# Performance work log

Measured on AMD Instinct MI355X. Metric: run time of the kernel, lower is better.

## Reference

```python
import jax, jax.numpy as jnp
import numpy as np

N6 = 524288          # nodes at depth 6 (full-octree batch of 2)
N5 = N6 // 8         # 65536 nodes at depth 5
N4 = N5 // 8         # 8192 nodes at depth 4
EPS = 1e-5           # torch BatchNorm1d default eps


def _pool(x):
    # octree_max_pool on a full octree: 8 contiguous children -> parent max
    n, c = x.shape
    return jnp.max(x.reshape(n // 8, 8, c), axis=1)


def _up(x):
    # octree_upsample on a full octree: each parent broadcast to its 8 children
    return jnp.repeat(x, 8, axis=0)


def _conv1x1_bn_relu(x, w, g, b):
    # Conv1x1 (Linear, no bias) + BatchNorm1d (training-mode batch stats) + ReLU
    y = x @ w                              # [N, Cout]
    m = jnp.mean(y, axis=0)
    v = jnp.var(y, axis=0)                 # biased variance, as in torch BN
    y = (y - m) * jax.lax.rsqrt(v + EPS) * g + b
    return jax.nn.relu(y)


def setup_inputs() -> dict:
    key = jax.random.key(0)
    ks = jax.random.split(key, 8)
    s = 0.02
    return {
        "data0": jax.random.normal(ks[0], (N6, 96), jnp.float32),
        "data1": jax.random.normal(ks[1], (N5, 192), jnp.float32),
        "w01": jax.random.normal(ks[2], (96, 192), jnp.float32) * s,
        "g01": jnp.ones((192,), jnp.float32),
        "b01": jnp.zeros((192,), jnp.float32),
        "w02": jax.random.normal(ks[3], (96, 384), jnp.float32) * s,
        "g02": jnp.ones((384,), jnp.float32),
        "b02": jnp.zeros((384,), jnp.float32),
        "w10": jax.random.normal(ks[4], (192, 96), jnp.float32) * s,
        "g10": jnp.ones((96,), jnp.float32),
        "b10": jnp.zeros((96,), jnp.float32),
        "w12": jax.random.normal(ks[5], (192, 384), jnp.float32) * s,
        "g12": jnp.ones((384,), jnp.float32),
        "b12": jnp.zeros((384,), jnp.float32),
        "depth": 6,
    }


def reference(data0, data1, w01, g01, b01, w02, g02, b02,
              w10, g10, b10, w12, g12, b12, depth):
    # channels = [96, 192, 384]; data0 at depth, data1 at depth-1.
    # out[j] = sum_i TransFunc(channels[i]->channels[j])(data[i], depth-i -> depth-j)
    # j=0 (depth, 96ch):   identity(data0) + upsample(conv10(data1))
    out0 = data0 + _up(_conv1x1_bn_relu(data1, w10, g10, b10))
    # j=1 (depth-1, 192ch): conv01(pool(data0)) + identity(data1)
    p0 = _pool(data0)                      # [N5, 96]
    out1 = _conv1x1_bn_relu(p0, w01, g01, b01) + data1
    # j=2 (depth-2, 384ch): conv02(pool^2(data0)) + conv12(pool(data1))
    out2 = (_conv1x1_bn_relu(_pool(p0), w02, g02, b02)
            + _conv1x1_bn_relu(_pool(data1), w12, g12, b12))
    return (out0, out1, out2)
```

## Files before the change

kernel.cpp:

```cpp
#include <hip/hip_runtime.h>

typedef unsigned short u16;
typedef __attribute__((ext_vector_type(8))) short short8;
typedef __attribute__((ext_vector_type(4))) float f4;
typedef __attribute__((ext_vector_type(4))) unsigned short u16x4;

#define CN6 524288
#define CN5 65536
#define CN4 8192

__device__ inline u16 f2bf(float f){
  unsigned u = __float_as_uint(f);
  return (u16)((u + 0x7FFFu + ((u >> 16) & 1u)) >> 16);
}
__device__ inline float bf2f(u16 h){ return __uint_as_float(((unsigned)h) << 16); }

__device__ inline f4 nt_load4(const float* p){
  return __builtin_nontemporal_load(reinterpret_cast<const f4*>(p));
}
__device__ inline void nt_store4(float* p, f4 v){
  __builtin_nontemporal_store(v, reinterpret_cast<f4*>(p));
}


__global__ __launch_bounds__(256) void k_prep(const float* __restrict__ w10, const float* __restrict__ w01,
                                              const float* __restrict__ w02, const float* __restrict__ w12,
                                              u16* __restrict__ wT10, u16* __restrict__ wT01,
                                              u16* __restrict__ wT02, u16* __restrict__ wT12,
                                              float* __restrict__ stats){
  int i = blockIdx.x * 256 + threadIdx.x;
  if (i < 2112) stats[i] = 0.f;
  if (i < 18432){ int j = i / 192, k = i - j * 192; wT10[i] = f2bf(w10[k * 96 + j]); }
  else if (i < 36864){ int e = i - 18432; int j = e / 96, k = e - j * 96; wT01[e] = f2bf(w01[k * 192 + j]); }
  else if (i < 73728){ int e = i - 36864; int j = e / 96, k = e - j * 96; wT02[e] = f2bf(w02[k * 384 + j]); }
  else if (i < 147456){ int e = i - 73728; int j = e / 192, k = e - j * 192; wT12[e] = f2bf(w12[k * 384 + j]); }
}

__global__ __launch_bounds__(256) void k_gemm10p(const float* __restrict__ d1, const u16* __restrict__ wT10,
                                                 u16* __restrict__ y10, u16* __restrict__ p1){
  __shared__ u16 sm[64 * 200];
  int tid = threadIdx.x, bid = blockIdx.x;

  if (tid < 192){
    int p = tid / 24, c8 = tid - p * 24;
    f4 v0[8], v1[8];
    #pragma unroll
    for (int r = 0; r < 8; r++){
      const float* src = d1 + ((size_t)bid * 64 + p * 8 + r) * 192 + c8 * 8;
      v0[r] = *reinterpret_cast<const f4*>(src);
      v1[r] = *reinterpret_cast<const f4*>(src + 4);
    }
    float mx[8];
    #pragma unroll
    for (int q = 0; q < 4; q++){ mx[q] = v0[0][q]; mx[4 + q] = v1[0][q]; }
    #pragma unroll
    for (int r = 0; r < 8; r++){
      short8 h;
      #pragma unroll
      for (int q = 0; q < 4; q++){
        h[q]     = (short)f2bf(v0[r][q]);
        h[4 + q] = (short)f2bf(v1[r][q]);
        if (r){ mx[q] = fmaxf(mx[q], v0[r][q]); mx[4 + q] = fmaxf(mx[4 + q], v1[r][q]); }
      }
      *reinterpret_cast<short8*>(&sm[(p * 8 + r) * 200 + c8 * 8]) = h;
    }
    short8 hp;
    #pragma unroll
    for (int q = 0; q < 8; q++) hp[q] = (short)f2bf(mx[q]);
    *reinterpret_cast<short8*>(p1 + ((size_t)bid * 8 + p) * 192 + c8 * 8) = hp;
  }
  __syncthreads();

  int lane = tid & 63, wave = tid >> 6;
  int colb = lane & 15;
  int k0 = (lane >> 4) * 8, rgrp = (lane >> 4) * 4;
  int arowl = wave * 16 + colb;
  short8 xf[6];
  #pragma unroll
  for (int s = 0; s < 6; s++) xf[s] = *reinterpret_cast<short8*>(&sm[arowl * 200 + s * 32 + k0]);

  size_t xrow = (size_t)bid * 64 + arowl;
  #pragma unroll
  for (int j = 0; j < 6; j++){
    f4 acc = {0.f, 0.f, 0.f, 0.f};
    const u16* wr = wT10 + (size_t)(j * 16 + colb) * 192 + k0;
    #pragma unroll
    for (int s = 0; s < 6; s++)
      acc = __builtin_amdgcn_mfma_f32_16x16x32_bf16(*reinterpret_cast<const short8*>(wr + s * 32), xf[s], acc, 0, 0, 0);
    u16x4 h;
    #pragma unroll
    for (int r = 0; r < 4; r++) h[r] = f2bf(acc[r]);
    *reinterpret_cast<u16x4*>(y10 + xrow * 96 + j * 16 + rgrp) = h;
  }
}

__global__ __launch_bounds__(192) void k_stats10(const u16* __restrict__ y10, float* __restrict__ stats){
  __shared__ float ls[96], lq[96];
  int tid = threadIdx.x, bid = blockIdx.x;
  if (tid < 96){ ls[tid] = 0.f; lq[tid] = 0.f; }
  __syncthreads();
  int c8 = tid % 12, rl = tid / 12;
  float s1[8], s2[8];
  #pragma unroll
  for (int q = 0; q < 8; q++){ s1[q] = 0.f; s2[q] = 0.f; }
  for (int it = 0; it < 32; it++){
    size_t row = (size_t)bid * 512 + it * 16 + rl;
    short8 h = *reinterpret_cast<const short8*>(y10 + row * 96 + c8 * 8);
    #pragma unroll
    for (int q = 0; q < 8; q++){
      float v = bf2f((u16)h[q]);
      s1[q] += v; s2[q] += v * v;
    }
  }
  #pragma unroll
  for (int q = 0; q < 8; q++){
    atomicAdd(&ls[c8 * 8 + q], s1[q]);
    atomicAdd(&lq[c8 * 8 + q], s2[q]);
  }
  __syncthreads();
  if (tid < 96){ atomicAdd(&stats[tid], ls[tid]); atomicAdd(&stats[1056 + tid], lq[tid]); }
}

__global__ __launch_bounds__(192) void k_out0(const float* __restrict__ d0, const u16* __restrict__ y10,
                                              const float* __restrict__ stats,
                                              const float* __restrict__ g10, const float* __restrict__ b10,
                                              float* __restrict__ out0, u16* __restrict__ p0, u16* __restrict__ p00){
  __shared__ float aL[96], cL[96];
  __shared__ float sp[8][96];
  int tid = threadIdx.x, gp = blockIdx.x;
  if (tid < 96){
    float m = stats[tid] * (1.f / 65536.f);
    float v = stats[1056 + tid] * (1.f / 65536.f) - m * m;
    float a = g10[tid] * rsqrtf(v + 1e-5f);
    aL[tid] = a; cL[tid] = b10[tid] - m * a;
  }
  __syncthreads();

  int p = tid / 24, c4 = tid - p * 24;
  int par = gp * 8 + p;
  u16x4 yb = *reinterpret_cast<const u16x4*>(y10 + (size_t)par * 96 + c4 * 4);
  size_t base = ((size_t)par * 8) * 96 + c4 * 4;

  f4 v[8];
  #pragma unroll
  for (int r = 0; r < 8; r++) v[r] = nt_load4(d0 + base + r * 96);

  f4 yv;
  #pragma unroll
  for (int q = 0; q < 4; q++){
    int c = c4 * 4 + q;
    yv[q] = fmaxf(bf2f((u16)yb[q]) * aL[c] + cL[c], 0.f);
  }
  f4 mx = v[0];
  #pragma unroll
  for (int r = 1; r < 8; r++)
    #pragma unroll
    for (int q = 0; q < 4; q++) mx[q] = fmaxf(mx[q], v[r][q]);

  #pragma unroll
  for (int r = 0; r < 8; r++){
    f4 o;
    #pragma unroll
    for (int q = 0; q < 4; q++) o[q] = v[r][q] + yv[q];
    nt_store4(out0 + base + r * 96, o);
  }

  u16x4 hp;
  #pragma unroll
  for (int q = 0; q < 4; q++) hp[q] = f2bf(mx[q]);
  *reinterpret_cast<u16x4*>(p0 + (size_t)par * 96 + c4 * 4) = hp;
  *reinterpret_cast<f4*>(&sp[p][c4 * 4]) = mx;
  __syncthreads();

  if (tid < 24){
    f4 m = *reinterpret_cast<f4*>(&sp[0][tid * 4]);
    #pragma unroll
    for (int pp = 1; pp < 8; pp++){
      f4 x = *reinterpret_cast<f4*>(&sp[pp][tid * 4]);
      #pragma unroll
      for (int q = 0; q < 4; q++) m[q] = fmaxf(m[q], x[q]);
    }
    u16x4 h;
    #pragma unroll
    for (int q = 0; q < 4; q++) h[q] = f2bf(m[q]);
    *reinterpret_cast<u16x4*>(p00 + (size_t)gp * 96 + tid * 4) = h;
  }
}

template<int Ci, int Co>
__device__ __forceinline__ void stats_body(const u16* __restrict__ x, const u16* __restrict__ wT,
                                           float* __restrict__ sum, float* __restrict__ sq,
                                           int bid, float* ls, float* lq){
  int tid = threadIdx.x;
  for (int t = tid; t < Co; t += 256){ ls[t] = 0.f; lq[t] = 0.f; }
  __syncthreads();
  int lane = tid & 63, wave = tid >> 6;
  int arow = bid * 64 + wave * 16 + (lane & 15);
  int k0 = (lane >> 4) * 8;
  constexpr int KS = Ci / 32;
  short8 af[KS];
  const u16* xr = x + (size_t)arow * Ci + k0;
  #pragma unroll
  for (int s = 0; s < KS; s++) af[s] = *reinterpret_cast<const short8*>(xr + s * 32);
  int colb = lane & 15;
  #pragma unroll 4
  for (int j = 0; j < Co / 16; j++){
    int col = j * 16 + colb;
    f4 acc = {0.f, 0.f, 0.f, 0.f};
    const u16* wr = wT + (size_t)col * Ci + k0;
    #pragma unroll
    for (int s = 0; s < KS; s++)
      acc = __builtin_amdgcn_mfma_f32_16x16x32_bf16(af[s], *reinterpret_cast<const short8*>(wr + s * 32), acc, 0, 0, 0);
    float s1 = acc[0] + acc[1] + acc[2] + acc[3];
    float s2 = acc[0]*acc[0] + acc[1]*acc[1] + acc[2]*acc[2] + acc[3]*acc[3];
    atomicAdd(&ls[col], s1);
    atomicAdd(&lq[col], s2);
  }
  __syncthreads();
  for (int t = tid; t < Co; t += 256){ atomicAdd(&sum[t], ls[t]); atomicAdd(&sq[t], lq[t]); }
}

__global__ __launch_bounds__(256) void k_statsAll(const u16* __restrict__ p0, const u16* __restrict__ p00,
                                                  const u16* __restrict__ p1,
                                                  const u16* __restrict__ wT01, const u16* __restrict__ wT02,
                                                  const u16* __restrict__ wT12, float* __restrict__ stats){
  __shared__ float ls[384], lq[384];
  int bid = blockIdx.x;
  if (bid < 1024)      stats_body<96, 192>(p0,  wT01, stats + 96,  stats + 1056 + 96,  bid,        ls, lq);
  else if (bid < 1152) stats_body<96, 384>(p00, wT02, stats + 288, stats + 1056 + 288, bid - 1024, ls, lq);
  else                 stats_body<192,384>(p1,  wT12, stats + 672, stats + 1056 + 672, bid - 1152, ls, lq);
}

__global__ __launch_bounds__(256) void k_out1(const u16* __restrict__ p0, const u16* __restrict__ wT01,
                                              const float* __restrict__ d1, const float* __restrict__ stats,
                                              const float* __restrict__ g01, const float* __restrict__ b01,
                                              float* __restrict__ out1){
  __shared__ float aL[192], cL[192];
  __shared__ float so[64 * 196];
  int tid = threadIdx.x, bid = blockIdx.x;
  if (tid < 192){
    float m = stats[96 + tid] * (1.f / 65536.f);
    float v = stats[1056 + 96 + tid] * (1.f / 65536.f) - m * m;
    float a = g01[tid] * rsqrtf(v + 1e-5f);
    aL[tid] = a; cL[tid] = b01[tid] - m * a;
  }
  __syncthreads();
  int lane = tid & 63, wave = tid >> 6;
  int colb = lane & 15;
  int k0 = (lane >> 4) * 8, rgrp = (lane >> 4) * 4;
  int rowl = wave * 16 + colb;
  short8 xf[3];
  const u16* xr = p0 + ((size_t)bid * 64 + rowl) * 96 + k0;
  #pragma unroll
  for (int s = 0; s < 3; s++) xf[s] = *reinterpret_cast<const short8*>(xr + s * 32);
  #pragma unroll 4
  for (int j = 0; j < 12; j++){
    int ch0 = j * 16 + rgrp;
    f4 acc = {0.f, 0.f, 0.f, 0.f};
    const u16* wr = wT01 + (size_t)(j * 16 + colb) * 96 + k0;
    #pragma unroll
    for (int s = 0; s < 3; s++)
      acc = __builtin_amdgcn_mfma_f32_16x16x32_bf16(*reinterpret_cast<const short8*>(wr + s * 32), xf[s], acc, 0, 0, 0);
    f4 o;
    #pragma unroll
    for (int r = 0; r < 4; r++){
      int ch = ch0 + r;
      o[r] = fmaxf(acc[r] * aL[ch] + cL[ch], 0.f);
    }
    *reinterpret_cast<f4*>(&so[rowl * 196 + ch0]) = o;
  }
  __syncthreads();
  const float* d1b = d1 + (size_t)bid * 64 * 192;
  float* o1b = out1 + (size_t)bid * 64 * 192;
  #pragma unroll
  for (int i = 0; i < 12; i++){
    int idx = i * 256 + tid;
    int rl = idx / 48, c4 = idx % 48;
    f4 y = *reinterpret_cast<f4*>(&so[rl * 196 + c4 * 4]);
    int off = rl * 192 + c4 * 4;
    f4 g = nt_load4(d1b + off);
    f4 o;
    #pragma unroll
    for (int q = 0; q < 4; q++) o[q] = y[q] + g[q];
    nt_store4(o1b + off, o);
  }
}

__global__ __launch_bounds__(256) void k_out2(const u16* __restrict__ p00, const u16* __restrict__ p1,
                                              const u16* __restrict__ wT02, const u16* __restrict__ wT12,
                                              const float* __restrict__ stats,
                                              const float* __restrict__ g02, const float* __restrict__ b02,
                                              const float* __restrict__ g12, const float* __restrict__ b12,
                                              float* __restrict__ out2){
  __shared__ float a2[384], c2[384], a1[384], c1[384];
  __shared__ float so[32 * 392];
  int tid = threadIdx.x, bid = blockIdx.x;
  for (int t = tid; t < 384; t += 256){
    float m = stats[288 + t] * (1.f / 8192.f);
    float v = stats[1056 + 288 + t] * (1.f / 8192.f) - m * m;
    float a = g02[t] * rsqrtf(v + 1e-5f);
    a2[t] = a; c2[t] = b02[t] - m * a;
    m = stats[672 + t] * (1.f / 8192.f);
    v = stats[1056 + 672 + t] * (1.f / 8192.f) - m * m;
    a = g12[t] * rsqrtf(v + 1e-5f);
    a1[t] = a; c1[t] = b12[t] - m * a;
  }
  __syncthreads();
  int lane = tid & 63, wave = tid >> 6;
  int wr2 = wave >> 1, wc = wave & 1;
  int colb = lane & 15;
  int k0 = (lane >> 4) * 8, rgrp = (lane >> 4) * 4;
  int rowl = wr2 * 16 + colb;
  size_t arow = (size_t)bid * 32 + rowl;
  short8 xA[3], xB[6];
  #pragma unroll
  for (int s = 0; s < 3; s++) xA[s] = *reinterpret_cast<const short8*>(p00 + arow * 96 + k0 + s * 32);
  #pragma unroll
  for (int s = 0; s < 6; s++) xB[s] = *reinterpret_cast<const short8*>(p1 + arow * 192 + k0 + s * 32);
  #pragma unroll 2
  for (int j = 0; j < 12; j++){
    int ch0 = wc * 192 + j * 16 + rgrp;
    int wrow = wc * 192 + j * 16 + colb;
    f4 u = {0.f, 0.f, 0.f, 0.f}, w = {0.f, 0.f, 0.f, 0.f};
    const u16* wra = wT02 + (size_t)wrow * 96 + k0;
    #pragma unroll
    for (int s = 0; s < 3; s++)
      u = __builtin_amdgcn_mfma_f32_16x16x32_bf16(*reinterpret_cast<const short8*>(wra + s * 32), xA[s], u, 0, 0, 0);
    const u16* wrb = wT12 + (size_t)wrow * 192 + k0;
    #pragma unroll
    for (int s = 0; s < 6; s++)
      w = __builtin_amdgcn_mfma_f32_16x16x32_bf16(*reinterpret_cast<const short8*>(wrb + s * 32), xB[s], w, 0, 0, 0);
    f4 o;
    #pragma unroll
    for (int r = 0; r < 4; r++){
      int ch = ch0 + r;
      o[r] = fmaxf(u[r] * a2[ch] + c2[ch], 0.f) + fmaxf(w[r] * a1[ch] + c1[ch], 0.f);
    }
    *reinterpret_cast<f4*>(&so[rowl * 392 + ch0]) = o;
  }
  __syncthreads();
  #pragma unroll
  for (int i = 0; i < 12; i++){
    int idx = i * 256 + tid;
    int rl = idx / 96, c4 = idx % 96;
    f4 v = *reinterpret_cast<f4*>(&so[rl * 392 + c4 * 4]);
    nt_store4(out2 + ((size_t)bid * 32 + rl) * 384 + c4 * 4, v);
  }
}

extern "C" void kernel_launch(void* const* d_in, const int* in_sizes, int n_in,
                              void* d_out, int out_size, void* d_ws, size_t ws_size,
                              hipStream_t stream){
  const float* data0 = (const float*)d_in[0];
  const float* data1 = (const float*)d_in[1];
  const float* w01 = (const float*)d_in[2];
  const float* g01 = (const float*)d_in[3];
  const float* b01 = (const float*)d_in[4];
  const float* w02 = (const float*)d_in[5];
  const float* g02 = (const float*)d_in[6];
  const float* b02 = (const float*)d_in[7];
  const float* w10 = (const float*)d_in[8];
  const float* g10 = (const float*)d_in[9];
  const float* b10 = (const float*)d_in[10];
  const float* w12 = (const float*)d_in[11];
  const float* g12 = (const float*)d_in[12];
  const float* b12 = (const float*)d_in[13];

  float* out0 = (float*)d_out;
  float* out1 = out0 + (size_t)CN6 * 96;
  float* out2 = out1 + (size_t)CN5 * 192;

  char* ws = (char*)d_ws;
  u16* p1   = (u16*)(ws + 0);
  u16* p0   = (u16*)(ws + 3145728);
  u16* p00  = (u16*)(ws + 15728640);
  u16* y10  = (u16*)(ws + 17301504);
  u16* wT10 = (u16*)(ws + 29884416);
  u16* wT01 = (u16*)(ws + 29921280);
  u16* wT02 = (u16*)(ws + 29958144);
  u16* wT12 = (u16*)(ws + 30031872);
  float* stats = (float*)(ws + 30179328);

  k_prep<<<576, 256, 0, stream>>>(w10, w01, w02, w12, wT10, wT01, wT02, wT12, stats);
  k_gemm10p<<<1024, 256, 0, stream>>>(data1, wT10, y10, p1);
  k_stats10<<<128, 192, 0, stream>>>(y10, stats);
  k_out0<<<8192, 192, 0, stream>>>(data0, y10, stats, g10, b10, out0, p0, p00);
  k_statsAll<<<1280, 256, 0, stream>>>(p0, p00, p1, wT01, wT02, wT12, stats);
  k_out1<<<1024, 256, 0, stream>>>(p0, wT01, data1, stats, g01, b01, out1);
  k_out2<<<256, 256, 0, stream>>>(p00, p1, wT02, wT12, stats, g02, b02, g12, b12, out2);
}
```

Baseline: 215.0 us.

## Fuse all stages into one persistent kernel with software grid barriers

Replaces the seven separate kernel launches with one persistent kernel of 256 blocks of 512 threads. The stages are separated by an atomic-counter grid barrier, and each stage uses grid-stride loops over its tiles. Shared memory is reused across stages through a union, and the per-stage tiling is reshaped to suit 512-thread blocks. This removes launch gaps and tail effects between stages. In exchange it adds barrier spin costs, depends on all 256 blocks being co-resident, and runs the large bandwidth-bound out0 stage with fewer blocks in flight.

```diff
diff --git a/kernel.cpp b/kernel.cpp
--- a/kernel.cpp
+++ b/kernel.cpp
@@ -8,6 +8,8 @@
 #define CN6 524288
 #define CN5 65536
 #define CN4 8192
+#define NBLK 256
+#define NTHR 512
 
 __device__ inline u16 f2bf(float f){
   unsigned u = __float_as_uint(f);
@@ -22,180 +24,42 @@
   __builtin_nontemporal_store(v, reinterpret_cast<f4*>(p));
 }
 
-
-__global__ __launch_bounds__(256) void k_prep(const float* __restrict__ w10, const float* __restrict__ w01,
-                                              const float* __restrict__ w02, const float* __restrict__ w12,
-                                              u16* __restrict__ wT10, u16* __restrict__ wT01,
-                                              u16* __restrict__ wT02, u16* __restrict__ wT12,
-                                              float* __restrict__ stats){
-  int i = blockIdx.x * 256 + threadIdx.x;
-  if (i < 2112) stats[i] = 0.f;
-  if (i < 18432){ int j = i / 192, k = i - j * 192; wT10[i] = f2bf(w10[k * 96 + j]); }
-  else if (i < 36864){ int e = i - 18432; int j = e / 96, k = e - j * 96; wT01[e] = f2bf(w01[k * 192 + j]); }
-  else if (i < 73728){ int e = i - 36864; int j = e / 96, k = e - j * 96; wT02[e] = f2bf(w02[k * 384 + j]); }
-  else if (i < 147456){ int e = i - 73728; int j = e / 192, k = e - j * 192; wT12[e] = f2bf(w12[k * 384 + j]); }
-}
-
-__global__ __launch_bounds__(256) void k_gemm10p(const float* __restrict__ d1, const u16* __restrict__ wT10,
-                                                 u16* __restrict__ y10, u16* __restrict__ p1){
-  __shared__ u16 sm[64 * 200];
-  int tid = threadIdx.x, bid = blockIdx.x;
-
-  if (tid < 192){
-    int p = tid / 24, c8 = tid - p * 24;
-    f4 v0[8], v1[8];
-    #pragma unroll
-    for (int r = 0; r < 8; r++){
-      const float* src = d1 + ((size_t)bid * 64 + p * 8 + r) * 192 + c8 * 8;
-      v0[r] = *reinterpret_cast<const f4*>(src);
-      v1[r] = *reinterpret_cast<const f4*>(src + 4);
-    }
-    float mx[8];
-    #pragma unroll
-    for (int q = 0; q < 4; q++){ mx[q] = v0[0][q]; mx[4 + q] = v1[0][q]; }
-    #pragma unroll
-    for (int r = 0; r < 8; r++){
-      short8 h;
-      #pragma unroll
-      for (int q = 0; q < 4; q++){
-        h[q]     = (short)f2bf(v0[r][q]);
-        h[4 + q] = (short)f2bf(v1[r][q]);
-        if (r){ mx[q] = fmaxf(mx[q], v0[r][q]); mx[4 + q] = fmaxf(mx[4 + q], v1[r][q]); }
-      }
-      *reinterpret_cast<short8*>(&sm[(p * 8 + r) * 200 + c8 * 8]) = h;
-    }
-    short8 hp;
-    #pragma unroll
-    for (int q = 0; q < 8; q++) hp[q] = (short)f2bf(mx[q]);
-    *reinterpret_cast<short8*>(p1 + ((size_t)bid * 8 + p) * 192 + c8 * 8) = hp;
-  }
-  __syncthreads();
-
+__device__ inline void gsync(unsigned* cnt, unsigned* gen){
+  __syncthreads();
+  if (threadIdx.x == 0){
+    __threadfence();
+    unsigned g = __hip_atomic_load(gen, __ATOMIC_RELAXED, __HIP_MEMORY_SCOPE_AGENT);
+    unsigned a = __hip_atomic_fetch_add(cnt, 1u, __ATOMIC_ACQ_REL, __HIP_MEMORY_SCOPE_AGENT);
+    if (a == NBLK - 1u){
+      __hip_atomic_store(cnt, 0u, __ATOMIC_RELAXED, __HIP_MEMORY_SCOPE_AGENT);
+      __hip_atomic_store(gen, g + 1u, __ATOMIC_RELEASE, __HIP_MEMORY_SCOPE_AGENT);
+    } else {
+      while (__hip_atomic_load(gen, __ATOMIC_ACQUIRE, __HIP_MEMORY_SCOPE_AGENT) == g)
+        __builtin_amdgcn_s_sleep(4);
+    }
+  }
+  __syncthreads();
+}
+
+union ShU {
+  struct { u16 sm[128 * 200]; } gm;
+  struct { float ls[96], lq[96]; } s10;
+  struct { float sp[16][96]; } o0;
+  struct { float ls[384], lq[384]; } sa;
+  struct { float aL[192], cL[192], so[64 * 196]; } o1;
+  struct { float a2[384], c2[384], a1[384], c1[384], so2[32 * 392]; } o2;
+};
+
+template<int Ci, int Co>
+__device__ __forceinline__ void sbody(const u16* __restrict__ x, const u16* __restrict__ wT,
+                                      float* __restrict__ sum, float* __restrict__ sq,
+                                      int pair, float* ls, float* lq){
+  int tid = threadIdx.x;
+  for (int t = tid; t < Co; t += NTHR){ ls[t] = 0.f; lq[t] = 0.f; }
+  __syncthreads();
   int lane = tid & 63, wave = tid >> 6;
-  int colb = lane & 15;
-  int k0 = (lane >> 4) * 8, rgrp = (lane >> 4) * 4;
-  int arowl = wave * 16 + colb;
-  short8 xf[6];
-  #pragma unroll
-  for (int s = 0; s < 6; s++) xf[s] = *reinterpret_cast<short8*>(&sm[arowl * 200 + s * 32 + k0]);
-
-  size_t xrow = (size_t)bid * 64 + arowl;
-  #pragma unroll
-  for (int j = 0; j < 6; j++){
-    f4 acc = {0.f, 0.f, 0.f, 0.f};
-    const u16* wr = wT10 + (size_t)(j * 16 + colb) * 192 + k0;
-    #pragma unroll
-    for (int s = 0; s < 6; s++)
-      acc = __builtin_amdgcn_mfma_f32_16x16x32_bf16(*reinterpret_cast<const short8*>(wr + s * 32), xf[s], acc, 0, 0, 0);
-    u16x4 h;
-    #pragma unroll
-    for (int r = 0; r < 4; r++) h[r] = f2bf(acc[r]);
-    *reinterpret_cast<u16x4*>(y10 + xrow * 96 + j * 16 + rgrp) = h;
-  }
-}
-
-__global__ __launch_bounds__(192) void k_stats10(const u16* __restrict__ y10, float* __restrict__ stats){
-  __shared__ float ls[96], lq[96];
-  int tid = threadIdx.x, bid = blockIdx.x;
-  if (tid < 96){ ls[tid] = 0.f; lq[tid] = 0.f; }
-  __syncthreads();
-  int c8 = tid % 12, rl = tid / 12;
-  float s1[8], s2[8];
-  #pragma unroll
-  for (int q = 0; q < 8; q++){ s1[q] = 0.f; s2[q] = 0.f; }
-  for (int it = 0; it < 32; it++){
-    size_t row = (size_t)bid * 512 + it * 16 + rl;
-    short8 h = *reinterpret_cast<const short8*>(y10 + row * 96 + c8 * 8);
-    #pragma unroll
-    for (int q = 0; q < 8; q++){
-      float v = bf2f((u16)h[q]);
-      s1[q] += v; s2[q] += v * v;
-    }
-  }
-  #pragma unroll
-  for (int q = 0; q < 8; q++){
-    atomicAdd(&ls[c8 * 8 + q], s1[q]);
-    atomicAdd(&lq[c8 * 8 + q], s2[q]);
-  }
-  __syncthreads();
-  if (tid < 96){ atomicAdd(&stats[tid], ls[tid]); atomicAdd(&stats[1056 + tid], lq[tid]); }
-}
-
-__global__ __launch_bounds__(192) void k_out0(const float* __restrict__ d0, const u16* __restrict__ y10,
-                                              const float* __restrict__ stats,
-                                              const float* __restrict__ g10, const float* __restrict__ b10,
-                                              float* __restrict__ out0, u16* __restrict__ p0, u16* __restrict__ p00){
-  __shared__ float aL[96], cL[96];
-  __shared__ float sp[8][96];
-  int tid = threadIdx.x, gp = blockIdx.x;
-  if (tid < 96){
-    float m = stats[tid] * (1.f / 65536.f);
-    float v = stats[1056 + tid] * (1.f / 65536.f) - m * m;
-    float a = g10[tid] * rsqrtf(v + 1e-5f);
-    aL[tid] = a; cL[tid] = b10[tid] - m * a;
-  }
-  __syncthreads();
-
-  int p = tid / 24, c4 = tid - p * 24;
-  int par = gp * 8 + p;
-  u16x4 yb = *reinterpret_cast<const u16x4*>(y10 + (size_t)par * 96 + c4 * 4);
-  size_t base = ((size_t)par * 8) * 96 + c4 * 4;
-
-  f4 v[8];
-  #pragma unroll
-  for (int r = 0; r < 8; r++) v[r] = nt_load4(d0 + base + r * 96);
-
-  f4 yv;
-  #pragma unroll
-  for (int q = 0; q < 4; q++){
-    int c = c4 * 4 + q;
-    yv[q] = fmaxf(bf2f((u16)yb[q]) * aL[c] + cL[c], 0.f);
-  }
-  f4 mx = v[0];
-  #pragma unroll
-  for (int r = 1; r < 8; r++)
-    #pragma unroll
-    for (int q = 0; q < 4; q++) mx[q] = fmaxf(mx[q], v[r][q]);
-
-  #pragma unroll
-  for (int r = 0; r < 8; r++){
-    f4 o;
-    #pragma unroll
-    for (int q = 0; q < 4; q++) o[q] = v[r][q] + yv[q];
-    nt_store4(out0 + base + r * 96, o);
-  }
-
-  u16x4 hp;
-  #pragma unroll
-  for (int q = 0; q < 4; q++) hp[q] = f2bf(mx[q]);
-  *reinterpret_cast<u16x4*>(p0 + (size_t)par * 96 + c4 * 4) = hp;
-  *reinterpret_cast<f4*>(&sp[p][c4 * 4]) = mx;
-  __syncthreads();
-
-  if (tid < 24){
-    f4 m = *reinterpret_cast<f4*>(&sp[0][tid * 4]);
-    #pragma unroll
-    for (int pp = 1; pp < 8; pp++){
-      f4 x = *reinterpret_cast<f4*>(&sp[pp][tid * 4]);
-      #pragma unroll
-      for (int q = 0; q < 4; q++) m[q] = fmaxf(m[q], x[q]);
-    }
-    u16x4 h;
-    #pragma unroll
-    for (int q = 0; q < 4; q++) h[q] = f2bf(m[q]);
-    *reinterpret_cast<u16x4*>(p00 + (size_t)gp * 96 + tid * 4) = h;
-  }
-}
-
-template<int Ci, int Co>
-__device__ __forceinline__ void stats_body(const u16* __restrict__ x, const u16* __restrict__ wT,
-                                           float* __restrict__ sum, float* __restrict__ sq,
-                                           int bid, float* ls, float* lq){
-  int tid = threadIdx.x;
-  for (int t = tid; t < Co; t += 256){ ls[t] = 0.f; lq[t] = 0.f; }
-  __syncthreads();
-  int lane = tid & 63, wave = tid >> 6;
-  int arow = bid * 64 + wave * 16 + (lane & 15);
+  int tile = pair * 2 + (wave >> 2);
+  int arow = tile * 64 + (wave & 3) * 16 + (lane & 15);
   int k0 = (lane >> 4) * 8;
   constexpr int KS = Ci / 32;
   short8 af[KS];
@@ -217,134 +81,291 @@
     atomicAdd(&lq[col], s2);
   }
   __syncthreads();
-  for (int t = tid; t < Co; t += 256){ atomicAdd(&sum[t], ls[t]); atomicAdd(&sq[t], lq[t]); }
-}
-
-__global__ __launch_bounds__(256) void k_statsAll(const u16* __restrict__ p0, const u16* __restrict__ p00,
-                                                  const u16* __restrict__ p1,
-                                                  const u16* __restrict__ wT01, const u16* __restrict__ wT02,
-                                                  const u16* __restrict__ wT12, float* __restrict__ stats){
-  __shared__ float ls[384], lq[384];
-  int bid = blockIdx.x;
-  if (bid < 1024)      stats_body<96, 192>(p0,  wT01, stats + 96,  stats + 1056 + 96,  bid,        ls, lq);
-  else if (bid < 1152) stats_body<96, 384>(p00, wT02, stats + 288, stats + 1056 + 288, bid - 1024, ls, lq);
-  else                 stats_body<192,384>(p1,  wT12, stats + 672, stats + 1056 + 672, bid - 1152, ls, lq);
-}
-
-__global__ __launch_bounds__(256) void k_out1(const u16* __restrict__ p0, const u16* __restrict__ wT01,
-                                              const float* __restrict__ d1, const float* __restrict__ stats,
-                                              const float* __restrict__ g01, const float* __restrict__ b01,
-                                              float* __restrict__ out1){
-  __shared__ float aL[192], cL[192];
-  __shared__ float so[64 * 196];
+  for (int t = tid; t < Co; t += NTHR){ atomicAdd(&sum[t], ls[t]); atomicAdd(&sq[t], lq[t]); }
+  __syncthreads();
+}
+
+__global__ __launch_bounds__(NTHR, 2) void mega(
+    const float* __restrict__ d0, const float* __restrict__ d1,
+    const float* __restrict__ w01, const float* __restrict__ g01, const float* __restrict__ b01,
+    const float* __restrict__ w02, const float* __restrict__ g02, const float* __restrict__ b02,
+    const float* __restrict__ w10, const float* __restrict__ g10, const float* __restrict__ b10,
+    const float* __restrict__ w12, const float* __restrict__ g12, const float* __restrict__ b12,
+    float* __restrict__ out0, float* __restrict__ out1, float* __restrict__ out2,
+    u16* __restrict__ p1, u16* __restrict__ p0, u16* __restrict__ p00, u16* __restrict__ y10,
+    u16* __restrict__ wT10, u16* __restrict__ wT01, u16* __restrict__ wT02, u16* __restrict__ wT12,
+    float* __restrict__ stats, unsigned* __restrict__ bar){
+  __shared__ ShU sh;
   int tid = threadIdx.x, bid = blockIdx.x;
+
+  for (int i = bid * NTHR + tid; i < 147456; i += NBLK * NTHR){
+    if (i < 2112) stats[i] = 0.f;
+    if (i < 18432){ int j = i / 192, k = i - j * 192; wT10[i] = f2bf(w10[k * 96 + j]); }
+    else if (i < 36864){ int e = i - 18432; int j = e / 96, k = e - j * 96; wT01[e] = f2bf(w01[k * 192 + j]); }
+    else if (i < 73728){ int e = i - 36864; int j = e / 96, k = e - j * 96; wT02[e] = f2bf(w02[k * 384 + j]); }
+    else { int e = i - 73728; int j = e / 192, k = e - j * 192; wT12[e] = f2bf(w12[k * 384 + j]); }
+  }
+  gsync(bar, bar + 1);
+
+  for (int dt = bid; dt < 512; dt += NBLK){
+    if (tid < 384){
+      int p = tid / 24, c8 = tid - p * 24;
+      f4 v0[8], v1[8];
+      #pragma unroll
+      for (int r = 0; r < 8; r++){
+        const float* src = d1 + ((size_t)dt * 128 + p * 8 + r) * 192 + c8 * 8;
+        v0[r] = *reinterpret_cast<const f4*>(src);
+        v1[r] = *reinterpret_cast<const f4*>(src + 4);
+      }
+      float mx[8];
+      #pragma unroll
+      for (int q = 0; q < 4; q++){ mx[q] = v0[0][q]; mx[4 + q] = v1[0][q]; }
+      #pragma unroll
+      for (int r = 0; r < 8; r++){
+        short8 h;
+        #pragma unroll
+        for (int q = 0; q < 4; q++){
+          h[q]     = (short)f2bf(v0[r][q]);
+          h[4 + q] = (short)f2bf(v1[r][q]);
+          if (r){ mx[q] = fmaxf(mx[q], v0[r][q]); mx[4 + q] = fmaxf(mx[4 + q], v1[r][q]); }
+        }
+        *reinterpret_cast<short8*>(&sh.gm.sm[(p * 8 + r) * 200 + c8 * 8]) = h;
+      }
+      short8 hp;
+      #pragma unroll
+      for (int q = 0; q < 8; q++) hp[q] = (short)f2bf(mx[q]);
+      *reinterpret_cast<short8*>(p1 + ((size_t)dt * 16 + p) * 192 + c8 * 8) = hp;
+    }
+    __syncthreads();
+    int lane = tid & 63, wave = tid >> 6;
+    int colb = lane & 15;
+    int k0 = (lane >> 4) * 8, rgrp = (lane >> 4) * 4;
+    int arowl = wave * 16 + colb;
+    short8 xf[6];
+    #pragma unroll
+    for (int s = 0; s < 6; s++) xf[s] = *reinterpret_cast<short8*>(&sh.gm.sm[arowl * 200 + s * 32 + k0]);
+    size_t xrow = (size_t)dt * 128 + arowl;
+    #pragma unroll
+    for (int j = 0; j < 6; j++){
+      f4 acc = {0.f, 0.f, 0.f, 0.f};
+      const u16* wr = wT10 + (size_t)(j * 16 + colb) * 192 + k0;
+      #pragma unroll
+      for (int s = 0; s < 6; s++)
+        acc = __builtin_amdgcn_mfma_f32_16x16x32_bf16(*reinterpret_cast<const short8*>(wr + s * 32), xf[s], acc, 0, 0, 0);
+      u16x4 h;
+      #pragma unroll
+      for (int r = 0; r < 4; r++) h[r] = f2bf(acc[r]);
+      *reinterpret_cast<u16x4*>(y10 + xrow * 96 + j * 16 + rgrp) = h;
+    }
+    __syncthreads();
+  }
+  gsync(bar, bar + 1);
+
+  for (int t = bid; t < 256; t += NBLK){
+    if (tid < 96){ sh.s10.ls[tid] = 0.f; sh.s10.lq[tid] = 0.f; }
+    __syncthreads();
+    if (tid < 384){
+      int c8 = tid % 12, rl = tid / 12;
+      float s1[8], s2[8];
+      #pragma unroll
+      for (int q = 0; q < 8; q++){ s1[q] = 0.f; s2[q] = 0.f; }
+      for (int it = 0; it < 8; it++){
+        size_t row = (size_t)t * 256 + it * 32 + rl;
+        short8 h = *reinterpret_cast<const short8*>(y10 + row * 96 + c8 * 8);
+        #pragma unroll
+        for (int q = 0; q < 8; q++){
+          float v = bf2f((u16)h[q]);
+          s1[q] += v; s2[q] += v * v;
+        }
+      }
+      #pragma unroll
+      for (int q = 0; q < 8; q++){
+        atomicAdd(&sh.s10.ls[c8 * 8 + q], s1[q]);
+        atomicAdd(&sh.s10.lq[c8 * 8 + q], s2[q]);
+      }
+    }
+    __syncthreads();
+    if (tid < 96){ atomicAdd(&stats[tid], sh.s10.ls[tid]); atomicAdd(&stats[1056 + tid], sh.s10.lq[tid]); }
+    __syncthreads();
+  }
+  gsync(bar, bar + 1);
+
+  {
+    int p2 = tid / 24, c4 = tid - p2 * 24;
+    float aR[4], cR[4];
+    if (tid < 384){
+      #pragma unroll
+      for (int q = 0; q < 4; q++){
+        int c = c4 * 4 + q;
+        float m = stats[c] * (1.f / 65536.f);
+        float v = stats[1056 + c] * (1.f / 65536.f) - m * m;
+        float a = g10[c] * rsqrtf(v + 1e-5f);
+        aR[q] = a; cR[q] = b10[c] - m * a;
+      }
+    }
+    for (int gp2 = bid; gp2 < 4096; gp2 += NBLK){
+      if (tid < 384){
+        int par = gp2 * 16 + p2;
+        u16x4 yb = *reinterpret_cast<const u16x4*>(y10 + (size_t)par * 96 + c4 * 4);
+        size_t base = ((size_t)par * 8) * 96 + c4 * 4;
+        f4 v[8];
+        #pragma unroll
+        for (int r = 0; r < 8; r++) v[r] = nt_load4(d0 + base + r * 96);
+        f4 yv;
+        #pragma unroll
+        for (int q = 0; q < 4; q++)
+          yv[q] = fmaxf(bf2f((u16)yb[q]) * aR[q] + cR[q], 0.f);
+        f4 mx = v[0];
+        #pragma unroll
+        for (int r = 1; r < 8; r++)
+          #pragma unroll
+          for (int q = 0; q < 4; q++) mx[q] = fmaxf(mx[q], v[r][q]);
+        #pragma unroll
+        for (int r = 0; r < 8; r++){
+          f4 o;
+          #pragma unroll
+          for (int q = 0; q < 4; q++) o[q] = v[r][q] + yv[q];
+          nt_store4(out0 + base + r * 96, o);
+        }
+        u16x4 hp;
+        #pragma unroll
+        for (int q = 0; q < 4; q++) hp[q] = f2bf(mx[q]);
+        *reinterpret_cast<u16x4*>(p0 + (size_t)par * 96 + c4 * 4) = hp;
+        *reinterpret_cast<f4*>(&sh.o0.sp[p2][c4 * 4]) = mx;
+      }
+      __syncthreads();
+      if (tid < 48){
+        int gpi = tid / 24, c4i = tid - gpi * 24;
+        f4 m = *reinterpret_cast<f4*>(&sh.o0.sp[gpi * 8][c4i * 4]);
+        #pragma unroll
+        for (int pp = 1; pp < 8; pp++){
+          f4 x = *reinterpret_cast<f4*>(&sh.o0.sp[gpi * 8 + pp][c4i * 4]);
+          #pragma unroll
+          for (int q = 0; q < 4; q++) m[q] = fmaxf(m[q], x[q]);
+        }
+        u16x4 h;
+        #pragma unroll
+        for (int q = 0; q < 4; q++) h[q] = f2bf(m[q]);
+        *reinterpret_cast<u16x4*>(p00 + (size_t)(gp2 * 2 + gpi) * 96 + c4i * 4) = h;
+      }
+      __syncthreads();
+    }
+  }
+  gsync(bar, bar + 1);
+
+  for (int t = bid; t < 640; t += NBLK){
+    if (t < 512)      sbody<96, 192>(p0,  wT01, stats + 96,  stats + 1056 + 96,  t,       sh.sa.ls, sh.sa.lq);
+    else if (t < 576) sbody<96, 384>(p00, wT02, stats + 288, stats + 1056 + 288, t - 512, sh.sa.ls, sh.sa.lq);
+    else              sbody<192,384>(p1,  wT12, stats + 672, stats + 1056 + 672, t - 576, sh.sa.ls, sh.sa.lq);
+  }
+  gsync(bar, bar + 1);
+
   if (tid < 192){
     float m = stats[96 + tid] * (1.f / 65536.f);
     float v = stats[1056 + 96 + tid] * (1.f / 65536.f) - m * m;
     float a = g01[tid] * rsqrtf(v + 1e-5f);
-    aL[tid] = a; cL[tid] = b01[tid] - m * a;
-  }
-  __syncthreads();
-  int lane = tid & 63, wave = tid >> 6;
-  int colb = lane & 15;
-  int k0 = (lane >> 4) * 8, rgrp = (lane >> 4) * 4;
-  int rowl = wave * 16 + colb;
-  short8 xf[3];
-  const u16* xr = p0 + ((size_t)bid * 64 + rowl) * 96 + k0;
-  #pragma unroll
-  for (int s = 0; s < 3; s++) xf[s] = *reinterpret_cast<const short8*>(xr + s * 32);
-  #pragma unroll 4
-  for (int j = 0; j < 12; j++){
-    int ch0 = j * 16 + rgrp;
-    f4 acc = {0.f, 0.f, 0.f, 0.f};
-    const u16* wr = wT01 + (size_t)(j * 16 + colb) * 96 + k0;
-    #pragma unroll
-    for (int s = 0; s < 3; s++)
-      acc = __builtin_amdgcn_mfma_f32_16x16x32_bf16(*reinterpret_cast<const short8*>(wr + s * 32), xf[s], acc, 0, 0, 0);
-    f4 o;
-    #pragma unroll
-    for (int r = 0; r < 4; r++){
-      int ch = ch0 + r;
-      o[r] = fmaxf(acc[r] * aL[ch] + cL[ch], 0.f);
-    }
-    *reinterpret_cast<f4*>(&so[rowl * 196 + ch0]) = o;
-  }
-  __syncthreads();
-  const float* d1b = d1 + (size_t)bid * 64 * 192;
-  float* o1b = out1 + (size_t)bid * 64 * 192;
-  #pragma unroll
-  for (int i = 0; i < 12; i++){
-    int idx = i * 256 + tid;
-    int rl = idx / 48, c4 = idx % 48;
-    f4 y = *reinterpret_cast<f4*>(&so[rl * 196 + c4 * 4]);
-    int off = rl * 192 + c4 * 4;
-    f4 g = nt_load4(d1b + off);
-    f4 o;
-    #pragma unroll
-    for (int q = 0; q < 4; q++) o[q] = y[q] + g[q];
-    nt_store4(o1b + off, o);
-  }
-}
-
-__global__ __launch_bounds__(256) void k_out2(const u16* __restrict__ p00, const u16* __restrict__ p1,
-                                              const u16* __restrict__ wT02, const u16* __restrict__ wT12,
-                                              const float* __restrict__ stats,
-                                              const float* __restrict__ g02, const float* __restrict__ b02,
-                                              const float* __restrict__ g12, const float* __restrict__ b12,
-                                              float* __restrict__ out2){
-  __shared__ float a2[384], c2[384], a1[384], c1[384];
-  __shared__ float so[32 * 392];
-  int tid = threadIdx.x, bid = blockIdx.x;
-  for (int t = tid; t < 384; t += 256){
-    float m = stats[288 + t] * (1.f / 8192.f);
-    float v = stats[1056 + 288 + t] * (1.f / 8192.f) - m * m;
-    float a = g02[t] * rsqrtf(v + 1e-5f);
-    a2[t] = a; c2[t] = b02[t] - m * a;
-    m = stats[672 + t] * (1.f / 8192.f);
-    v = stats[1056 + 672 + t] * (1.f / 8192.f) - m * m;
-    a = g12[t] * rsqrtf(v + 1e-5f);
-    a1[t] = a; c1[t] = b12[t] - m * a;
-  }
-  __syncthreads();
-  int lane = tid & 63, wave = tid >> 6;
-  int wr2 = wave >> 1, wc = wave & 1;
-  int colb = lane & 15;
-  int k0 = (lane >> 4) * 8, rgrp = (lane >> 4) * 4;
-  int rowl = wr2 * 16 + colb;
-  size_t arow = (size_t)bid * 32 + rowl;
-  short8 xA[3], xB[6];
-  #pragma unroll
-  for (int s = 0; s < 3; s++) xA[s] = *reinterpret_cast<const short8*>(p00 + arow * 96 + k0 + s * 32);
-  #pragma unroll
-  for (int s = 0; s < 6; s++) xB[s] = *reinterpret_cast<const short8*>(p1 + arow * 192 + k0 + s * 32);
-  #pragma unroll 2
-  for (int j = 0; j < 12; j++){
-    int ch0 = wc * 192 + j * 16 + rgrp;
-    int wrow = wc * 192 + j * 16 + colb;
-    f4 u = {0.f, 0.f, 0.f, 0.f}, w = {0.f, 0.f, 0.f, 0.f};
-    const u16* wra = wT02 + (size_t)wrow * 96 + k0;
-    #pragma unroll
-    for (int s = 0; s < 3; s++)
-      u = __builtin_amdgcn_mfma_f32_16x16x32_bf16(*reinterpret_cast<const short8*>(wra + s * 32), xA[s], u, 0, 0, 0);
-    const u16* wrb = wT12 + (size_t)wrow * 192 + k0;
-    #pragma unroll
-    for (int s = 0; s < 6; s++)
-      w = __builtin_amdgcn_mfma_f32_16x16x32_bf16(*reinterpret_cast<const short8*>(wrb + s * 32), xB[s], w, 0, 0, 0);
-    f4 o;
-    #pragma unroll
-    for (int r = 0; r < 4; r++){
-      int ch = ch0 + r;
-      o[r] = fmaxf(u[r] * a2[ch] + c2[ch], 0.f) + fmaxf(w[r] * a1[ch] + c1[ch], 0.f);
-    }
-    *reinterpret_cast<f4*>(&so[rowl * 392 + ch0]) = o;
-  }
-  __syncthreads();
-  #pragma unroll
-  for (int i = 0; i < 12; i++){
-    int idx = i * 256 + tid;
-    int rl = idx / 96, c4 = idx % 96;
-    f4 v = *reinterpret_cast<f4*>(&so[rl * 392 + c4 * 4]);
-    nt_store4(out2 + ((size_t)bid * 32 + rl) * 384 + c4 * 4, v);
+    sh.o1.aL[tid] = a; sh.o1.cL[tid] = b01[tid] - m * a;
+  }
+  __syncthreads();
+  for (int t = bid; t < 1024; t += NBLK){
+    int lane = tid & 63, wave = tid >> 6;
+    int colb = lane & 15;
+    int k0 = (lane >> 4) * 8, rgrp = (lane >> 4) * 4;
+    int jg = wave >> 2;
+    int rowl = (wave & 3) * 16 + colb;
+    short8 xf[3];
+    const u16* xr = p0 + ((size_t)t * 64 + rowl) * 96 + k0;
+    #pragma unroll
+    for (int s = 0; s < 3; s++) xf[s] = *reinterpret_cast<const short8*>(xr + s * 32);
+    #pragma unroll
+    for (int jj = 0; jj < 6; jj++){
+      int j = jg * 6 + jj;
+      int ch0 = j * 16 + rgrp;
+      f4 acc = {0.f, 0.f, 0.f, 0.f};
+      const u16* wr = wT01 + (size_t)(j * 16 + colb) * 96 + k0;
+      #pragma unroll
+      for (int s = 0; s < 3; s++)
+        acc = __builtin_amdgcn_mfma_f32_16x16x32_bf16(*reinterpret_cast<const short8*>(wr + s * 32), xf[s], acc, 0, 0, 0);
+      f4 o;
+      #pragma unroll
+      for (int r = 0; r < 4; r++){
+        int ch = ch0 + r;
+        o[r] = fmaxf(acc[r] * sh.o1.aL[ch] + sh.o1.cL[ch], 0.f);
+      }
+      *reinterpret_cast<f4*>(&sh.o1.so[rowl * 196 + ch0]) = o;
+    }
+    __syncthreads();
+    const float* d1b = d1 + (size_t)t * 64 * 192;
+    float* o1b = out1 + (size_t)t * 64 * 192;
+    #pragma unroll
+    for (int i = 0; i < 6; i++){
+      int idx = i * NTHR + tid;
+      int rl = idx / 48, c4i = idx % 48;
+      f4 y = *reinterpret_cast<f4*>(&sh.o1.so[rl * 196 + c4i * 4]);
+      int off = rl * 192 + c4i * 4;
+      f4 g = nt_load4(d1b + off);
+      f4 o;
+      #pragma unroll
+      for (int q = 0; q < 4; q++) o[q] = y[q] + g[q];
+      nt_store4(o1b + off, o);
+    }
+    __syncthreads();
+  }
+  __syncthreads();
+
+  if (tid < 384){
+    float m = stats[288 + tid] * (1.f / 8192.f);
+    float v = stats[1056 + 288 + tid] * (1.f / 8192.f) - m * m;
+    float a = g02[tid] * rsqrtf(v + 1e-5f);
+    sh.o2.a2[tid] = a; sh.o2.c2[tid] = b02[tid] - m * a;
+    m = stats[672 + tid] * (1.f / 8192.f);
+    v = stats[1056 + 672 + tid] * (1.f / 8192.f) - m * m;
+    a = g12[tid] * rsqrtf(v + 1e-5f);
+    sh.o2.a1[tid] = a; sh.o2.c1[tid] = b12[tid] - m * a;
+  }
+  __syncthreads();
+  for (int t = bid; t < 256; t += NBLK){
+    int lane = tid & 63, wave = tid >> 6;
+    int rowg = wave >> 2, colq = wave & 3;
+    int colb = lane & 15;
+    int k0 = (lane >> 4) * 8, rgrp = (lane >> 4) * 4;
+    int rowl = rowg * 16 + colb;
+    size_t arow = (size_t)t * 32 + rowl;
+    short8 xA[3], xB[6];
+    #pragma unroll
+    for (int s = 0; s < 3; s++) xA[s] = *reinterpret_cast<const short8*>(p00 + arow * 96 + k0 + s * 32);
+    #pragma unroll
+    for (int s = 0; s < 6; s++) xB[s] = *reinterpret_cast<const short8*>(p1 + arow * 192 + k0 + s * 32);
+    #pragma unroll
+    for (int j = 0; j < 6; j++){
+      int ch0 = colq * 96 + j * 16 + rgrp;
+      int wrow = colq * 96 + j * 16 + colb;
+      f4 u = {0.f, 0.f, 0.f, 0.f}, w = {0.f, 0.f, 0.f, 0.f};
+      const u16* wra = wT02 + (size_t)wrow * 96 + k0;
+      #pragma unroll
+      for (int s = 0; s < 3; s++)
+        u = __builtin_amdgcn_mfma_f32_16x16x32_bf16(*reinterpret_cast<const short8*>(wra + s * 32), xA[s], u, 0, 0, 0);
+      const u16* wrb = wT12 + (size_t)wrow * 192 + k0;
+      #pragma unroll
+      for (int s = 0; s < 6; s++)
+        w = __builtin_amdgcn_mfma_f32_16x16x32_bf16(*reinterpret_cast<const short8*>(wrb + s * 32), xB[s], w, 0, 0, 0);
+      f4 o;
+      #pragma unroll
+      for (int r = 0; r < 4; r++){
+        int ch = ch0 + r;
+        o[r] = fmaxf(u[r] * sh.o2.a2[ch] + sh.o2.c2[ch], 0.f) + fmaxf(w[r] * sh.o2.a1[ch] + sh.o2.c1[ch], 0.f);
+      }
+      *reinterpret_cast<f4*>(&sh.o2.so2[rowl * 392 + ch0]) = o;
+    }
+    __syncthreads();
+    #pragma unroll
+    for (int i = 0; i < 6; i++){
+      int idx = i * NTHR + tid;
+      int rl = idx / 96, c4i = idx % 96;
+      f4 v = *reinterpret_cast<f4*>(&sh.o2.so2[rl * 392 + c4i * 4]);
+      nt_store4(out2 + ((size_t)t * 32 + rl) * 384 + c4i * 4, v);
+    }
+    __syncthreads();
   }
 }
 
@@ -380,12 +401,10 @@
   u16* wT02 = (u16*)(ws + 29958144);
   u16* wT12 = (u16*)(ws + 30031872);
   float* stats = (float*)(ws + 30179328);
-
-  k_prep<<<576, 256, 0, stream>>>(w10, w01, w02, w12, wT10, wT01, wT02, wT12, stats);
-  k_gemm10p<<<1024, 256, 0, stream>>>(data1, wT10, y10, p1);
-  k_stats10<<<128, 192, 0, stream>>>(y10, stats);
-  k_out0<<<8192, 192, 0, stream>>>(data0, y10, stats, g10, b10, out0, p0, p00);
-  k_statsAll<<<1280, 256, 0, stream>>>(p0, p00, p1, wT01, wT02, wT12, stats);
-  k_out1<<<1024, 256, 0, stream>>>(p0, wT01, data1, stats, g01, b01, out1);
-  k_out2<<<256, 256, 0, stream>>>(p00, p1, wT02, wT12, stats, g02, b02, g12, b12, out2);
-}
+  unsigned* bar = (unsigned*)(ws + 30187776);
+
+  hipMemsetAsync(bar, 0, 8, stream);
+  mega<<<NBLK, NTHR, 0, stream>>>(data0, data1,
+      w01, g01, b01, w02, g02, b02, w10, g10, b10, w12, g12, b12,
+      out0, out1, out2, p1, p0, p00, y10, wT10, wT01, wT02, wT12, stats, bar);
+}
```

Result: slower. 423.7 us (+97.0%).

## Coalesce k_out0 data0 streaming via contiguous loads and LDS-staged pooling

Applied to the files above, without the earlier changes.

k_out0 now uses 256 threads that read and write the block's 6144-float tile of data0/out0 contiguously, instead of each thread striding across rows. Rows are staged in shared memory so the 8-child max-pool can be computed from LDS. The BN affine for y10 is now computed per thread directly from the stats, replacing the separate shared-memory setup pass. This targets memory coalescing on the largest tensor, at the cost of more LDS traffic, an extra barrier and higher LDS usage per block.

```diff
diff --git a/kernel.cpp b/kernel.cpp
--- a/kernel.cpp
+++ b/kernel.cpp
@@ -121,57 +121,66 @@
   if (tid < 96){ atomicAdd(&stats[tid], ls[tid]); atomicAdd(&stats[1056 + tid], lq[tid]); }
 }
 
-__global__ __launch_bounds__(192) void k_out0(const float* __restrict__ d0, const u16* __restrict__ y10,
+__global__ __launch_bounds__(256) void k_out0(const float* __restrict__ d0, const u16* __restrict__ y10,
                                               const float* __restrict__ stats,
                                               const float* __restrict__ g10, const float* __restrict__ b10,
                                               float* __restrict__ out0, u16* __restrict__ p0, u16* __restrict__ p00){
-  __shared__ float aL[96], cL[96];
+  __shared__ float yv[8][96];
+  __shared__ float sd[64][100];
   __shared__ float sp[8][96];
   int tid = threadIdx.x, gp = blockIdx.x;
-  if (tid < 96){
-    float m = stats[tid] * (1.f / 65536.f);
-    float v = stats[1056 + tid] * (1.f / 65536.f) - m * m;
-    float a = g10[tid] * rsqrtf(v + 1e-5f);
-    aL[tid] = a; cL[tid] = b10[tid] - m * a;
-  }
-  __syncthreads();
-
-  int p = tid / 24, c4 = tid - p * 24;
-  int par = gp * 8 + p;
-  u16x4 yb = *reinterpret_cast<const u16x4*>(y10 + (size_t)par * 96 + c4 * 4);
-  size_t base = ((size_t)par * 8) * 96 + c4 * 4;
-
-  f4 v[8];
-  #pragma unroll
-  for (int r = 0; r < 8; r++) v[r] = nt_load4(d0 + base + r * 96);
-
-  f4 yv;
-  #pragma unroll
-  for (int q = 0; q < 4; q++){
-    int c = c4 * 4 + q;
-    yv[q] = fmaxf(bf2f((u16)yb[q]) * aL[c] + cL[c], 0.f);
-  }
-  f4 mx = v[0];
-  #pragma unroll
-  for (int r = 1; r < 8; r++)
-    #pragma unroll
-    for (int q = 0; q < 4; q++) mx[q] = fmaxf(mx[q], v[r][q]);
-
-  #pragma unroll
-  for (int r = 0; r < 8; r++){
+
+  if (tid < 192){
+    int p = tid / 24, c4 = tid - p * 24;
+    u16x4 yb = *reinterpret_cast<const u16x4*>(y10 + ((size_t)gp * 8 + p) * 96 + c4 * 4);
     f4 o;
     #pragma unroll
-    for (int q = 0; q < 4; q++) o[q] = v[r][q] + yv[q];
-    nt_store4(out0 + base + r * 96, o);
-  }
-
-  u16x4 hp;
-  #pragma unroll
-  for (int q = 0; q < 4; q++) hp[q] = f2bf(mx[q]);
-  *reinterpret_cast<u16x4*>(p0 + (size_t)par * 96 + c4 * 4) = hp;
-  *reinterpret_cast<f4*>(&sp[p][c4 * 4]) = mx;
-  __syncthreads();
-
+    for (int q = 0; q < 4; q++){
+      int c = c4 * 4 + q;
+      float m = stats[c] * (1.f / 65536.f);
+      float vv = stats[1056 + c] * (1.f / 65536.f) - m * m;
+      float a = g10[c] * rsqrtf(vv + 1e-5f);
+      float cc = b10[c] - m * a;
+      o[q] = fmaxf(bf2f((u16)yb[q]) * a + cc, 0.f);
+    }
+    *reinterpret_cast<f4*>(&yv[p][c4 * 4]) = o;
+  }
+  __syncthreads();
+
+  const float* dsrc = d0 + (size_t)gp * 6144;
+  float* ddst = out0 + (size_t)gp * 6144;
+  f4 v[6];
+  #pragma unroll
+  for (int i = 0; i < 6; i++) v[i] = nt_load4(dsrc + (i * 256 + tid) * 4);
+  #pragma unroll
+  for (int i = 0; i < 6; i++){
+    int idx = i * 256 + tid;
+    int row = idx / 24, c4 = idx - row * 24;
+    f4 y = *reinterpret_cast<f4*>(&yv[row >> 3][c4 * 4]);
+    f4 o;
+    #pragma unroll
+    for (int q = 0; q < 4; q++) o[q] = v[i][q] + y[q];
+    nt_store4(ddst + idx * 4, o);
+    *reinterpret_cast<f4*>(&sd[row][c4 * 4]) = v[i];
+  }
+  __syncthreads();
+
+  if (tid < 192){
+    int p = tid / 24, c4 = tid - p * 24;
+    f4 m = *reinterpret_cast<f4*>(&sd[p * 8][c4 * 4]);
+    #pragma unroll
+    for (int r = 1; r < 8; r++){
+      f4 x = *reinterpret_cast<f4*>(&sd[p * 8 + r][c4 * 4]);
+      #pragma unroll
+      for (int q = 0; q < 4; q++) m[q] = fmaxf(m[q], x[q]);
+    }
+    u16x4 h;
+    #pragma unroll
+    for (int q = 0; q < 4; q++) h[q] = f2bf(m[q]);
+    *reinterpret_cast<u16x4*>(p0 + ((size_t)gp * 8 + p) * 96 + c4 * 4) = h;
+    *reinterpret_cast<f4*>(&sp[p][c4 * 4]) = m;
+  }
+  __syncthreads();
   if (tid < 24){
     f4 m = *reinterpret_cast<f4*>(&sp[0][tid * 4]);
     #pragma unroll
@@ -275,9 +284,9 @@
   #pragma unroll
   for (int i = 0; i < 12; i++){
     int idx = i * 256 + tid;
-    int rl = idx / 48, c4 = idx % 48;
-    f4 y = *reinterpret_cast<f4*>(&so[rl * 196 + c4 * 4]);
-    int off = rl * 192 + c4 * 4;
+    int rl = idx / 48, c4i = idx % 48;
+    f4 y = *reinterpret_cast<f4*>(&so[rl * 196 + c4i * 4]);
+    int off = rl * 192 + c4i * 4;
     f4 g = nt_load4(d1b + off);
     f4 o;
     #pragma unroll
@@ -342,9 +351,9 @@
   #pragma unroll
   for (int i = 0; i < 12; i++){
     int idx = i * 256 + tid;
-    int rl = idx / 96, c4 = idx % 96;
-    f4 v = *reinterpret_cast<f4*>(&so[rl * 392 + c4 * 4]);
-    nt_store4(out2 + ((size_t)bid * 32 + rl) * 384 + c4 * 4, v);
+    int rl = idx / 96, c4i = idx % 96;
+    f4 v = *reinterpret_cast<f4*>(&so[rl * 392 + c4i * 4]);
+    nt_store4(out2 + ((size_t)bid * 32 + rl) * 384 + c4i * 4, v);
   }
 }
 
@@ -384,7 +393,7 @@
   k_prep<<<576, 256, 0, stream>>>(w10, w01, w02, w12, wT10, wT01, wT02, wT12, stats);
   k_gemm10p<<<1024, 256, 0, stream>>>(data1, wT10, y10, p1);
   k_stats10<<<128, 192, 0, stream>>>(y10, stats);
-  k_out0<<<8192, 192, 0, stream>>>(data0, y10, stats, g10, b10, out0, p0, p00);
+  k_out0<<<8192, 256, 0, stream>>>(data0, y10, stats, g10, b10, out0, p0, p00);
   k_statsAll<<<1280, 256, 0, stream>>>(p0, p00, p1, wT01, wT02, wT12, stats);
   k_out1<<<1024, 256, 0, stream>>>(p0, wT01, data1, stats, g01, b01, out1);
   k_out2<<<256, 256, 0, stream>>>(p00, p1, wT02, wT12, stats, g02, b02, g12, b12, out2);
```

Result: no change. 213.8 us (-0.6%).
